# Optimization experiments

Measured on AMD Instinct MI355X. Metric: run time of the kernel, lower is better.

## Reference

```python
import jax, jax.numpy as jnp
import numpy as np

N = 100000
E = 1600000
F_IN, H = 64, 128


def setup_inputs() -> dict:
    key = jax.random.key(0)
    ks = jax.random.split(key, 8)
    inp = {
        "x": jax.random.normal(ks[0], (N, F_IN), dtype=jnp.float32),
        "edge_index": jax.random.randint(ks[1], (2, E), 0, N, dtype=jnp.int64),
        "W1": jax.random.normal(ks[2], (F_IN, H), dtype=jnp.float32) / np.sqrt(F_IN),
        "b1": jnp.zeros((H,), jnp.float32),
        "W2": jax.random.normal(ks[3], (H, H), dtype=jnp.float32) / np.sqrt(H),
        "b2": jnp.zeros((H,), jnp.float32),
        "W3": jax.random.normal(ks[4], (H, H // 2), dtype=jnp.float32) / np.sqrt(H),
        "b3": jnp.zeros((H // 2,), jnp.float32),
        "Wc1": jax.random.normal(ks[5], (H // 2, H // 4), dtype=jnp.float32) / np.sqrt(H // 2),
        "bc1": jnp.zeros((H // 4,), jnp.float32),
        "Wc2": jax.random.normal(ks[6], (H // 4, 2), dtype=jnp.float32) / np.sqrt(H // 4),
        "bc2": jnp.zeros((2,), jnp.float32),
    }
    return inp


def _gcn_norm(edge_index, n):
    # PyG GCNConv default: add self-loops, symmetric D^-1/2 A_hat D^-1/2 norm
    loop = jnp.arange(n, dtype=edge_index.dtype)
    src = jnp.concatenate([edge_index[0], loop])
    dst = jnp.concatenate([edge_index[1], loop])
    deg = jax.ops.segment_sum(jnp.ones_like(dst, dtype=jnp.float32), dst, num_segments=n)
    dis = jax.lax.rsqrt(jnp.maximum(deg, 1.0))
    norm = dis[src] * dis[dst]  # [E+N]
    return src, dst, norm


def _gcn_conv(x, W, b, src, dst, norm, n):
    h = x @ W                      # [N, H_out]
    msg = h[src] * norm[:, None]   # gather + scale, [E+N, H_out]
    out = jax.ops.segment_sum(msg, dst, num_segments=n)  # scatter-add
    return out + b


def reference(x, edge_index, W1, b1, W2, b2, W3, b3, Wc1, bc1, Wc2, bc2):
    n = x.shape[0]
    src, dst, norm = _gcn_norm(edge_index, n)
    h1 = jax.nn.relu(_gcn_conv(x, W1, b1, src, dst, norm, n))
    h2 = jax.nn.relu(_gcn_conv(h1, W2, b2, src, dst, norm, n))
    h3 = jax.nn.relu(_gcn_conv(h2, W3, b3, src, dst, norm, n))
    pooled = jnp.mean(h3, axis=0, keepdims=True)  # [1, H//2]
    z = jax.nn.relu(pooled @ Wc1 + bc1)
    logits = z @ Wc2 + bc2
    return jax.nn.softmax(logits, axis=1)
```

## Files before the change

### kernel.cpp

```cpp
#include <hip/hip_runtime.h>

#define NN 100000
#define NE 1600000
#define NBUCKET 391
#define CHUNK 4096

typedef __attribute__((ext_vector_type(2))) float v2f;
typedef __attribute__((ext_vector_type(8))) short bf16x8;
typedef __attribute__((ext_vector_type(4))) float f32x4;


__device__ __forceinline__ unsigned int pk4fp8(float a, float b, float c, float d) {
    int t = __builtin_amdgcn_cvt_pk_fp8_f32(a, b, 0, false);
    t = __builtin_amdgcn_cvt_pk_fp8_f32(c, d, t, true);
    return (unsigned int)t;
}
__device__ __forceinline__ void acc4(unsigned int u, float* a) {
    v2f p0 = __builtin_amdgcn_cvt_pk_f32_fp8((int)u, false);
    v2f p1 = __builtin_amdgcn_cvt_pk_f32_fp8((int)u, true);
    a[0] += p0.x; a[1] += p0.y; a[2] += p1.x; a[3] += p1.y;
}
__device__ __forceinline__ void acc16(uint4 u, float* a) {
    acc4(u.x, a); acc4(u.y, a + 4); acc4(u.z, a + 8); acc4(u.w, a + 12);
}


__device__ __forceinline__ unsigned short f2b(float f) {
    unsigned int u; __builtin_memcpy(&u, &f, 4);
    unsigned int r = (u + 0x7fffu + ((u >> 16) & 1u)) >> 16;
    return (unsigned short)r;
}
__device__ __forceinline__ unsigned int pk2b(float a, float b) {
    return (unsigned int)f2b(a) | ((unsigned int)f2b(b) << 16);
}

__global__ __launch_bounds__(256) void k_init(
    const float* __restrict__ W1, const float* __restrict__ W2,
    const float* __restrict__ W3, uint4* __restrict__ Wp,
    int* __restrict__ bcnt, int* __restrict__ done_cnt) {
    int t = blockIdx.x * 256 + threadIdx.x;
    if (t < 4096) {
        const float* W; int Dout, e, base;
        if (t < 1024)       { W = W1; Dout = 128; e = t;        base = 0; }
        else if (t < 3072)  { W = W2; Dout = 128; e = t - 1024; base = 1024; }
        else                { W = W3; Dout = 64;  e = t - 3072; base = 3072; }
        int k4q = e / Dout, ch = e % Dout;
        int k0 = (k4q >> 2) * 32 + (k4q & 3) * 8;
        float v[8];
        #pragma unroll
        for (int j = 0; j < 8; j++) v[j] = W[(k0 + j) * Dout + ch];
        uint4 u;
        u.x = pk2b(v[0], v[1]); u.y = pk2b(v[2], v[3]);
        u.z = pk2b(v[4], v[5]); u.w = pk2b(v[6], v[7]);
        Wp[base + e] = u;
    } else {
        int i = t - 4096;
        if (i < NBUCKET) bcnt[i] = 0;
        if (i == NBUCKET) { done_cnt[0] = 0; done_cnt[1] = 0; }
    }
}

__global__ __launch_bounds__(512) void k_p12(const int* __restrict__ dst,
                                             int* __restrict__ bcnt,
                                             int* __restrict__ bbase,
                                             int* __restrict__ bfill,
                                             int* __restrict__ done_cnt, int E) {
    __shared__ int h[NBUCKET];
    __shared__ int s[512];
    __shared__ int isLast;
    int t = threadIdx.x;
    for (int i = t; i < NBUCKET; i += 512) h[i] = 0;
    __syncthreads();
    int stride = gridDim.x * 512;
    for (int i = blockIdx.x * 512 + t; i < E; i += stride)
        atomicAdd(&h[dst[i] >> 8], 1);
    __syncthreads();
    for (int i = t; i < NBUCKET; i += 512)
        if (h[i]) atomicAdd(&bcnt[i], h[i]);
    __threadfence();
    if (t == 0) isLast = (atomicAdd(&done_cnt[0], 1) == (int)gridDim.x - 1);
    __syncthreads();
    if (!isLast) return;
    __threadfence();
    int v = (t < NBUCKET) ? bcnt[t] : 0;
    s[t] = v; __syncthreads();
    for (int off = 1; off < 512; off <<= 1) {
        int x = (t >= off) ? s[t - off] : 0;
        __syncthreads();
        s[t] += x;
        __syncthreads();
    }
    if (t < NBUCKET) { int ex = s[t] - v; bbase[t] = ex; bfill[t] = ex; }
    if (t == NBUCKET) bbase[t] = s[511];
}

__global__ __launch_bounds__(256) void k_p2(const int* __restrict__ src,
                                            const int* __restrict__ dst,
                                            int* __restrict__ bfill,
                                            unsigned int* __restrict__ entries, int E) {
    __shared__ int h[NBUCKET];
    __shared__ int cur[NBUCKET];
    int c0 = blockIdx.x * CHUNK;
    int c1 = min(E, c0 + CHUNK);
    for (int i = threadIdx.x; i < NBUCKET; i += 256) h[i] = 0;
    __syncthreads();
    for (int i = c0 + threadIdx.x; i < c1; i += 256) atomicAdd(&h[dst[i] >> 8], 1);
    __syncthreads();
    for (int i = threadIdx.x; i < NBUCKET; i += 256)
        cur[i] = h[i] ? atomicAdd(&bfill[i], h[i]) : 0;
    __syncthreads();
    for (int i = c0 + threadIdx.x; i < c1; i += 256) {
        int d = dst[i];
        int bkt = d >> 8;
        int pos = atomicAdd(&cur[bkt], 1);
        entries[pos] = (unsigned int)src[i] | ((unsigned int)(d & 255) << 17);
    }
}

__global__ __launch_bounds__(256) void k_p4x(const unsigned int* __restrict__ entries,
                                             const int* __restrict__ bbase,
                                             int* __restrict__ row_ptr,
                                             float* __restrict__ dis,
                                             int* __restrict__ col,
                                             const float4* __restrict__ x4,
                                             uint2* __restrict__ xb2, int N) {
    __shared__ int cnt[256];
    __shared__ int cur[256];
    __shared__ int sc[256];
    __shared__ float sdis[256];
    int b = blockIdx.x;
    int e0 = bbase[b], e1 = bbase[b + 1];
    int t = threadIdx.x;
    cnt[t] = 0; __syncthreads();
    for (int i = e0 + t; i < e1; i += 256)
        atomicAdd(&cnt[(entries[i] >> 17) & 255], 1);
    __syncthreads();
    int v = cnt[t];
    sc[t] = v; __syncthreads();
    for (int off = 1; off < 256; off <<= 1) {
        int x = (t >= off) ? sc[t - off] : 0;
        __syncthreads();
        sc[t] += x;
        __syncthreads();
    }
    int ex = sc[t] - v;
    int n = (b << 8) + t;
    float dv = rsqrtf((float)(v + 1));
    if (n <= N) row_ptr[n] = e0 + ex;
    if (n < N) dis[n] = dv;
    sdis[t] = dv;
    cur[t] = e0 + ex;
    __syncthreads();
    for (int i = e0 + t; i < e1; i += 256) {
        unsigned int en = entries[i];
        int pos = atomicAdd(&cur[(en >> 17) & 255], 1);
        col[pos] = (int)(en & 0x1FFFF);
    }
    for (int idx = t; idx < 256 * 8; idx += 256) {
        int node = idx >> 3, k = idx & 7;
        int gn = (b << 8) + node;
        if (gn < N) {
            float s = sdis[node];
            float4 A = x4[gn * 16 + 2 * k];
            float4 B = x4[gn * 16 + 2 * k + 1];
            uint2 u;
            u.x = pk4fp8(A.x * s, A.y * s, A.z * s, A.w * s);
            u.y = pk4fp8(B.x * s, B.y * s, B.z * s, B.w * s);
            xb2[gn * 8 + k] = u;
        }
    }
}

__global__ __launch_bounds__(256) void k_l1f(
    const uint4* __restrict__ xb4, const int* __restrict__ row_ptr,
    const int* __restrict__ col, const float* __restrict__ dis,
    const uint4* __restrict__ Wp, const float* __restrict__ b1,
    unsigned int* __restrict__ h1u, int N) {
    __shared__ unsigned short lds[4][16][72];
    const int tid = threadIdx.x, lane = tid & 63, wave = tid >> 6;
    const int slot = lane >> 2, seg = lane & 3;
    const int n = blockIdx.x * 64 + wave * 16 + slot;
    float a[16];
    #pragma unroll
    for (int q = 0; q < 16; q++) a[q] = 0.f;
    if (n < N) {
        int b = row_ptr[n], e = row_ptr[n + 1];
        acc16(xb4[n * 4 + seg], a);
        int i = b;
        for (; i + 4 <= e; i += 4) {
            int c0 = col[i], c1 = col[i + 1], c2 = col[i + 2], c3 = col[i + 3];
            uint4 u0 = xb4[c0 * 4 + seg], u1 = xb4[c1 * 4 + seg];
            uint4 u2 = xb4[c2 * 4 + seg], u3 = xb4[c3 * 4 + seg];
            acc16(u0, a); acc16(u1, a); acc16(u2, a); acc16(u3, a);
        }
        for (; i < e; i++) acc16(xb4[col[i] * 4 + seg], a);
        float s = dis[n];
        #pragma unroll
        for (int q = 0; q < 16; q++) a[q] *= s;
    }
    uint4 u0, u1;
    u0.x = pk2b(a[0],  a[1]);  u0.y = pk2b(a[2],  a[3]);
    u0.z = pk2b(a[4],  a[5]);  u0.w = pk2b(a[6],  a[7]);
    u1.x = pk2b(a[8],  a[9]);  u1.y = pk2b(a[10], a[11]);
    u1.z = pk2b(a[12], a[13]); u1.w = pk2b(a[14], a[15]);
    *(uint4*)&lds[wave][slot][seg * 16]     = u0;
    *(uint4*)&lds[wave][slot][seg * 16 + 8] = u1;
    __syncthreads();
    const int quad = lane >> 4, l16 = lane & 15;
    const int node = blockIdx.x * 64 + wave * 16 + l16;
    const bool valid = node < N;
    bf16x8 bfrag[2];
    #pragma unroll
    for (int kt = 0; kt < 2; kt++)
        bfrag[kt] = *(bf16x8*)&lds[wave][l16][kt * 32 + quad * 8];
    const float s2 = valid ? dis[node] : 0.f;
    #pragma unroll
    for (int ct = 0; ct < 8; ct++) {
        f32x4 c = {0.f, 0.f, 0.f, 0.f};
        #pragma unroll
        for (int kt = 0; kt < 2; kt++) {
            uint4 wu = Wp[(kt * 4 + quad) * 128 + ct * 16 + l16];
            c = __builtin_amdgcn_mfma_f32_16x16x32_bf16(*(bf16x8*)&wu, bfrag[kt], c, 0, 0, 0);
        }
        if (valid) {
            const int chb = ct * 16 + quad * 4;
            float r0 = fmaxf(c[0] + b1[chb + 0], 0.f) * s2;
            float r1 = fmaxf(c[1] + b1[chb + 1], 0.f) * s2;
            float r2 = fmaxf(c[2] + b1[chb + 2], 0.f) * s2;
            float r3 = fmaxf(c[3] + b1[chb + 3], 0.f) * s2;
            h1u[(size_t)node * 32 + ct * 4 + quad] = pk4fp8(r0, r1, r2, r3);
        }
    }
}

__global__ __launch_bounds__(256) void k_agg128s(
    const uint4* __restrict__ g4, const int* __restrict__ row_ptr,
    const int* __restrict__ col, const float* __restrict__ dis,
    uint4* __restrict__ outb, int N) {
    int tid = threadIdx.x;
    int lane = tid & 63, wave = tid >> 6;
    int slot = lane >> 3, seg = lane & 7;
    int n = blockIdx.x * 32 + wave * 8 + slot;
    if (n >= N) return;
    int b = row_ptr[n], e = row_ptr[n + 1];
    float a[16];
    #pragma unroll
    for (int q = 0; q < 16; q++) a[q] = 0.f;
    acc16(g4[n * 8 + seg], a);
    int i = b;
    for (; i + 4 <= e; i += 4) {
        int c0 = col[i], c1 = col[i + 1], c2 = col[i + 2], c3 = col[i + 3];
        uint4 u0 = g4[c0 * 8 + seg], u1 = g4[c1 * 8 + seg];
        uint4 u2 = g4[c2 * 8 + seg], u3 = g4[c3 * 8 + seg];
        acc16(u0, a); acc16(u1, a); acc16(u2, a); acc16(u3, a);
    }
    for (; i < e; i++) acc16(g4[col[i] * 8 + seg], a);
    float s = dis[n];
    uint4 u0, u1;
    u0.x = pk2b(s*a[0],  s*a[1]);  u0.y = pk2b(s*a[2],  s*a[3]);
    u0.z = pk2b(s*a[4],  s*a[5]);  u0.w = pk2b(s*a[6],  s*a[7]);
    u1.x = pk2b(s*a[8],  s*a[9]);  u1.y = pk2b(s*a[10], s*a[11]);
    u1.z = pk2b(s*a[12], s*a[13]); u1.w = pk2b(s*a[14], s*a[15]);
    outb[n * 16 + seg * 2]     = u0;
    outb[n * 16 + seg * 2 + 1] = u1;
}

__global__ __launch_bounds__(256) void k_mm23(
    const uint4* __restrict__ Xb,
    const uint4* __restrict__ Wp2, const uint4* __restrict__ Wp3,
    const float* __restrict__ b2, const float* __restrict__ dis,
    unsigned int* __restrict__ g3u, int N) {
    __shared__ unsigned short lds[4][16][136];
    const int tid = threadIdx.x, lane = tid & 63, wave = tid >> 6;
    const int quad = lane >> 4, l16 = lane & 15;
    const int node = blockIdx.x * 64 + wave * 16 + l16;
    const bool valid = node < N;
    const int nc = valid ? node : (N - 1);
    bf16x8 bfrag[4];
    const uint4* xrow = Xb + (size_t)nc * 16;
    #pragma unroll
    for (int kt = 0; kt < 4; kt++) {
        uint4 u = xrow[kt * 4 + quad];
        bfrag[kt] = *(bf16x8*)&u;
    }
    const float s = valid ? dis[node] : 0.f;
    #pragma unroll
    for (int ct = 0; ct < 8; ct++) {
        f32x4 c = {0.f, 0.f, 0.f, 0.f};
        #pragma unroll
        for (int kt = 0; kt < 4; kt++) {
            uint4 wu = Wp2[(kt * 4 + quad) * 128 + ct * 16 + l16];
            c = __builtin_amdgcn_mfma_f32_16x16x32_bf16(*(bf16x8*)&wu, bfrag[kt], c, 0, 0, 0);
        }
        const int chb = ct * 16 + quad * 4;
        float r0 = fmaxf(c[0] + b2[chb + 0], 0.f) * s;
        float r1 = fmaxf(c[1] + b2[chb + 1], 0.f) * s;
        float r2 = fmaxf(c[2] + b2[chb + 2], 0.f) * s;
        float r3 = fmaxf(c[3] + b2[chb + 3], 0.f) * s;
        uint2 u; u.x = pk2b(r0, r1); u.y = pk2b(r2, r3);
        *(uint2*)&lds[wave][l16][chb] = u;
    }
    __syncthreads();
    bf16x8 b2frag[4];
    #pragma unroll
    for (int kt = 0; kt < 4; kt++)
        b2frag[kt] = *(bf16x8*)&lds[wave][l16][kt * 32 + quad * 8];
    #pragma unroll
    for (int ct = 0; ct < 4; ct++) {
        f32x4 c = {0.f, 0.f, 0.f, 0.f};
        #pragma unroll
        for (int kt = 0; kt < 4; kt++) {
            uint4 wu = Wp3[(kt * 4 + quad) * 64 + ct * 16 + l16];
            c = __builtin_amdgcn_mfma_f32_16x16x32_bf16(*(bf16x8*)&wu, b2frag[kt], c, 0, 0, 0);
        }
        if (valid)
            g3u[(size_t)node * 16 + ct * 4 + quad] = pk4fp8(c[0], c[1], c[2], c[3]);
    }
}

__global__ __launch_bounds__(256) void k_aggpools(
    const uint4* __restrict__ g4, const int* __restrict__ row_ptr,
    const int* __restrict__ col, const float* __restrict__ dis,
    const float* __restrict__ b3, float* __restrict__ partial, int N) {
    int tid = threadIdx.x;
    int lane = tid & 63, wave = tid >> 6;
    int slot = lane >> 2, seg = lane & 3;
    int n = blockIdx.x * 64 + wave * 16 + slot;
    float ap[16];
    #pragma unroll
    for (int j = 0; j < 16; j++) ap[j] = 0.f;
    if (n < N) {
        int b = row_ptr[n], e = row_ptr[n + 1];
        float a[16];
        #pragma unroll
        for (int q = 0; q < 16; q++) a[q] = 0.f;
        acc16(g4[n * 4 + seg], a);
        int i = b;
        for (; i + 4 <= e; i += 4) {
            int c0 = col[i], c1 = col[i + 1], c2 = col[i + 2], c3 = col[i + 3];
            uint4 u0 = g4[c0 * 4 + seg], u1 = g4[c1 * 4 + seg];
            uint4 u2 = g4[c2 * 4 + seg], u3 = g4[c3 * 4 + seg];
            acc16(u0, a); acc16(u1, a); acc16(u2, a); acc16(u3, a);
        }
        for (; i < e; i++) acc16(g4[col[i] * 4 + seg], a);
        float s = dis[n];
        #pragma unroll
        for (int j = 0; j < 16; j++)
            ap[j] = fmaxf(s * a[j] + b3[seg * 16 + j], 0.f);
    }
    #pragma unroll
    for (int j = 0; j < 16; j++) {
        ap[j] += __shfl_xor(ap[j], 4);
        ap[j] += __shfl_xor(ap[j], 8);
        ap[j] += __shfl_xor(ap[j], 16);
        ap[j] += __shfl_xor(ap[j], 32);
    }
    __shared__ float red[4][64];
    if (slot == 0) {
        #pragma unroll
        for (int j = 0; j < 16; j++) red[wave][seg * 16 + j] = ap[j];
    }
    __syncthreads();
    if (tid < 64)
        partial[blockIdx.x * 64 + tid] =
            red[0][tid] + red[1][tid] + red[2][tid] + red[3][tid];
}

__global__ __launch_bounds__(256) void k_redhead(
    const float* __restrict__ partial, float* __restrict__ partial2,
    const float* __restrict__ Wc1, const float* __restrict__ bc1,
    const float* __restrict__ Wc2, const float* __restrict__ bc2,
    float* __restrict__ out, int* __restrict__ done_cnt,
    int NB, int NRED, float invN) {
    __shared__ float red[256];
    __shared__ float pooled[64];
    __shared__ float z[32];
    __shared__ float lg[2];
    __shared__ int isLast;
    int blk = blockIdx.x, t = threadIdx.x;
    int lane = t & 63, grp = t >> 6;
    int start = blk * 16, end = min(NB, start + 16);
    float s = 0.f;
    for (int b = start + grp; b < end; b += 4) s += partial[b * 64 + lane];
    red[t] = s; __syncthreads();
    if (t < 64)
        partial2[blk * 64 + t] = red[t] + red[t + 64] + red[t + 128] + red[t + 192];
    __threadfence();
    if (t == 0) isLast = (atomicAdd(done_cnt, 1) == NRED - 1);
    __syncthreads();
    if (!isLast) return;
    __threadfence();
    float s2 = 0.f;
    for (int b = grp; b < NRED; b += 4) s2 += partial2[b * 64 + lane];
    red[t] = s2; __syncthreads();
    if (t < 64) pooled[t] = (red[t] + red[t + 64] + red[t + 128] + red[t + 192]) * invN;
    __syncthreads();
    if (t < 32) {
        float a = bc1[t];
        for (int l = 0; l < 64; l++) a += pooled[l] * Wc1[l * 32 + t];
        z[t] = fmaxf(a, 0.f);
    }
    __syncthreads();
    if (t < 2) {
        float a = bc2[t];
        for (int j = 0; j < 32; j++) a += z[j] * Wc2[j * 2 + t];
        lg[t] = a;
    }
    __syncthreads();
    if (t == 0) {
        float m = fmaxf(lg[0], lg[1]);
        float e0 = __expf(lg[0] - m), e1 = __expf(lg[1] - m);
        float inv = 1.f / (e0 + e1);
        out[0] = e0 * inv;
        out[1] = e1 * inv;
    }
}


extern "C" void kernel_launch(void* const* d_in, const int* in_sizes, int n_in,
                              void* d_out, int out_size, void* d_ws, size_t ws_size,
                              hipStream_t stream) {
    (void)in_sizes; (void)n_in; (void)out_size; (void)ws_size;
    const int N = NN, E = NE;

    const float* x   = (const float*)d_in[0];
    const int*   ei  = (const int*)d_in[1];
    const int*   srcp = ei;
    const int*   dstp = ei + E;
    const float* W1 = (const float*)d_in[2];
    const float* b1 = (const float*)d_in[3];
    const float* W2 = (const float*)d_in[4];
    const float* b2 = (const float*)d_in[5];
    const float* W3 = (const float*)d_in[6];
    const float* b3 = (const float*)d_in[7];
    const float* Wc1 = (const float*)d_in[8];
    const float* bc1 = (const float*)d_in[9];
    const float* Wc2 = (const float*)d_in[10];
    const float* bc2 = (const float*)d_in[11];
    float* out = (float*)d_out;

    char* base = (char*)d_ws;
    size_t off = 0;
    auto carve = [&](size_t bytes) -> char* {
        char* p = base + off;
        off = (off + bytes + 255) & ~(size_t)255;
        return p;
    };
    int*   bcnt    = (int*)carve((size_t)NBUCKET * 4);
    int*   bbase   = (int*)carve((size_t)(NBUCKET + 1) * 4);
    int*   bfill   = (int*)carve((size_t)NBUCKET * 4);
    int*   done_cnt= (int*)carve(256);
    int*   row_ptr = (int*)carve((size_t)(N + 1) * 4);
    int*   col     = (int*)carve((size_t)E * 4);
    float* dis     = (float*)carve((size_t)N * 4);
    float* partial = (float*)carve((size_t)1600 * 64 * 4);
    float* partial2= (float*)carve((size_t)128 * 64 * 4);
    uint4* Wp      = (uint4*)carve((size_t)4096 * 16);
    unsigned int* entries = (unsigned int*)carve((size_t)E * 4);
    unsigned int* xb      = (unsigned int*)carve((size_t)N * 64);
    unsigned int* h1u     = (unsigned int*)carve((size_t)N * 128);
    unsigned int* g3u     = (unsigned int*)carve((size_t)N * 64);
    uint4*        bufB    = (uint4*)carve((size_t)N * 128 * 2);

    k_init<<<18, 256, 0, stream>>>(W1, W2, W3, Wp, bcnt, done_cnt);
    k_p12<<<256, 512, 0, stream>>>(dstp, bcnt, bbase, bfill, &done_cnt[0], E);
    k_p2<<<(E + CHUNK - 1) / CHUNK, 256, 0, stream>>>(srcp, dstp, bfill, entries, E);
    k_p4x<<<NBUCKET, 256, 0, stream>>>(entries, bbase, row_ptr, dis, col,
                                       (const float4*)x, (uint2*)xb, N);

    const int NB64 = (N + 63) / 64;
    const int NB32 = (N + 31) / 32;

    k_l1f<<<NB64, 256, 0, stream>>>((const uint4*)xb, row_ptr, col, dis, Wp, b1, h1u, N);

    k_agg128s<<<NB32, 256, 0, stream>>>((const uint4*)h1u, row_ptr, col, dis, bufB, N);
    k_mm23<<<NB64, 256, 0, stream>>>(bufB, Wp + 1024, Wp + 3072, b2, dis, g3u, N);

    k_aggpools<<<NB64, 256, 0, stream>>>((const uint4*)g3u, row_ptr, col, dis, b3, partial, N);

    const int NRED = (NB64 + 15) / 16;
    k_redhead<<<NRED, 256, 0, stream>>>(partial, partial2, Wc1, bc1, Wc2, bc2,
                                        out, &done_cnt[1], NB64, NRED, 1.0f / (float)N);
}
```

Baseline: 311.8 us.

## Fuse layer-2 aggregation into matmul kernel via LDS, split histogram/scan kernels

```diff
diff --git a/kernel.cpp b/kernel.cpp
--- a/kernel.cpp
+++ b/kernel.cpp
@@ -60,28 +60,24 @@
     }
 }
 
-__global__ __launch_bounds__(512) void k_p12(const int* __restrict__ dst,
-                                             int* __restrict__ bcnt,
-                                             int* __restrict__ bbase,
-                                             int* __restrict__ bfill,
-                                             int* __restrict__ done_cnt, int E) {
+
+__global__ __launch_bounds__(256) void k_p1(const int* __restrict__ dst,
+                                            int* __restrict__ bcnt, int E) {
     __shared__ int h[NBUCKET];
+    for (int i = threadIdx.x; i < NBUCKET; i += 256) h[i] = 0;
+    __syncthreads();
+    int stride = gridDim.x * 256;
+    for (int i = blockIdx.x * 256 + threadIdx.x; i < E; i += stride)
+        atomicAdd(&h[dst[i] >> 8], 1);
+    __syncthreads();
+    for (int i = threadIdx.x; i < NBUCKET; i += 256)
+        if (h[i]) atomicAdd(&bcnt[i], h[i]);
+}
+
+__global__ void k_scanb(const int* __restrict__ bcnt, int* __restrict__ bbase,
+                        int* __restrict__ bfill) {
     __shared__ int s[512];
-    __shared__ int isLast;
     int t = threadIdx.x;
-    for (int i = t; i < NBUCKET; i += 512) h[i] = 0;
-    __syncthreads();
-    int stride = gridDim.x * 512;
-    for (int i = blockIdx.x * 512 + t; i < E; i += stride)
-        atomicAdd(&h[dst[i] >> 8], 1);
-    __syncthreads();
-    for (int i = t; i < NBUCKET; i += 512)
-        if (h[i]) atomicAdd(&bcnt[i], h[i]);
-    __threadfence();
-    if (t == 0) isLast = (atomicAdd(&done_cnt[0], 1) == (int)gridDim.x - 1);
-    __syncthreads();
-    if (!isLast) return;
-    __threadfence();
     int v = (t < NBUCKET) ? bcnt[t] : 0;
     s[t] = v; __syncthreads();
     for (int off = 1; off < 512; off <<= 1) {
@@ -233,56 +229,54 @@
     }
 }
 
-__global__ __launch_bounds__(256) void k_agg128s(
-    const uint4* __restrict__ g4, const int* __restrict__ row_ptr,
+__global__ __launch_bounds__(256) void k_l2f(
+    const uint4* __restrict__ h1b4, const int* __restrict__ row_ptr,
     const int* __restrict__ col, const float* __restrict__ dis,
-    uint4* __restrict__ outb, int N) {
-    int tid = threadIdx.x;
-    int lane = tid & 63, wave = tid >> 6;
-    int slot = lane >> 3, seg = lane & 7;
-    int n = blockIdx.x * 32 + wave * 8 + slot;
-    if (n >= N) return;
-    int b = row_ptr[n], e = row_ptr[n + 1];
-    float a[16];
-    #pragma unroll
-    for (int q = 0; q < 16; q++) a[q] = 0.f;
-    acc16(g4[n * 8 + seg], a);
-    int i = b;
-    for (; i + 4 <= e; i += 4) {
-        int c0 = col[i], c1 = col[i + 1], c2 = col[i + 2], c3 = col[i + 3];
-        uint4 u0 = g4[c0 * 8 + seg], u1 = g4[c1 * 8 + seg];
-        uint4 u2 = g4[c2 * 8 + seg], u3 = g4[c3 * 8 + seg];
-        acc16(u0, a); acc16(u1, a); acc16(u2, a); acc16(u3, a);
-    }
-    for (; i < e; i++) acc16(g4[col[i] * 8 + seg], a);
-    float s = dis[n];
-    uint4 u0, u1;
-    u0.x = pk2b(s*a[0],  s*a[1]);  u0.y = pk2b(s*a[2],  s*a[3]);
-    u0.z = pk2b(s*a[4],  s*a[5]);  u0.w = pk2b(s*a[6],  s*a[7]);
-    u1.x = pk2b(s*a[8],  s*a[9]);  u1.y = pk2b(s*a[10], s*a[11]);
-    u1.z = pk2b(s*a[12], s*a[13]); u1.w = pk2b(s*a[14], s*a[15]);
-    outb[n * 16 + seg * 2]     = u0;
-    outb[n * 16 + seg * 2 + 1] = u1;
-}
-
-__global__ __launch_bounds__(256) void k_mm23(
-    const uint4* __restrict__ Xb,
     const uint4* __restrict__ Wp2, const uint4* __restrict__ Wp3,
-    const float* __restrict__ b2, const float* __restrict__ dis,
+    const float* __restrict__ b2,
     unsigned int* __restrict__ g3u, int N) {
     __shared__ unsigned short lds[4][16][136];
     const int tid = threadIdx.x, lane = tid & 63, wave = tid >> 6;
+    const int slot = lane >> 3, seg = lane & 7;
+    #pragma unroll
+    for (int j = 0; j < 2; j++) {
+        const int nl = wave * 16 + j * 8 + slot;
+        const int n = blockIdx.x * 64 + nl;
+        float a[16];
+        #pragma unroll
+        for (int q = 0; q < 16; q++) a[q] = 0.f;
+        if (n < N) {
+            int b = row_ptr[n], e = row_ptr[n + 1];
+            acc16(h1b4[(size_t)n * 8 + seg], a);
+            int i = b;
+            for (; i + 4 <= e; i += 4) {
+                int c0 = col[i], c1 = col[i + 1], c2 = col[i + 2], c3 = col[i + 3];
+                uint4 u0 = h1b4[(size_t)c0 * 8 + seg], u1 = h1b4[(size_t)c1 * 8 + seg];
+                uint4 u2 = h1b4[(size_t)c2 * 8 + seg], u3 = h1b4[(size_t)c3 * 8 + seg];
+                acc16(u0, a); acc16(u1, a); acc16(u2, a); acc16(u3, a);
+            }
+            for (; i < e; i++) acc16(h1b4[(size_t)col[i] * 8 + seg], a);
+            float s = dis[n];
+            #pragma unroll
+            for (int q = 0; q < 16; q++) a[q] *= s;
+        }
+        uint4 u0, u1;
+        u0.x = pk2b(a[0],  a[1]);  u0.y = pk2b(a[2],  a[3]);
+        u0.z = pk2b(a[4],  a[5]);  u0.w = pk2b(a[6],  a[7]);
+        u1.x = pk2b(a[8],  a[9]);  u1.y = pk2b(a[10], a[11]);
+        u1.z = pk2b(a[12], a[13]); u1.w = pk2b(a[14], a[15]);
+        const int lnl = j * 8 + slot;
+        *(uint4*)&lds[wave][lnl][seg * 16]     = u0;
+        *(uint4*)&lds[wave][lnl][seg * 16 + 8] = u1;
+    }
+    __syncthreads();
     const int quad = lane >> 4, l16 = lane & 15;
     const int node = blockIdx.x * 64 + wave * 16 + l16;
     const bool valid = node < N;
-    const int nc = valid ? node : (N - 1);
     bf16x8 bfrag[4];
-    const uint4* xrow = Xb + (size_t)nc * 16;
-    #pragma unroll
-    for (int kt = 0; kt < 4; kt++) {
-        uint4 u = xrow[kt * 4 + quad];
-        bfrag[kt] = *(bf16x8*)&u;
-    }
+    #pragma unroll
+    for (int kt = 0; kt < 4; kt++)
+        bfrag[kt] = *(bf16x8*)&lds[wave][l16][kt * 32 + quad * 8];
     const float s = valid ? dis[node] : 0.f;
     #pragma unroll
     for (int ct = 0; ct < 8; ct++) {
@@ -460,21 +454,20 @@
     unsigned int* xb      = (unsigned int*)carve((size_t)N * 64);
     unsigned int* h1u     = (unsigned int*)carve((size_t)N * 128);
     unsigned int* g3u     = (unsigned int*)carve((size_t)N * 64);
-    uint4*        bufB    = (uint4*)carve((size_t)N * 128 * 2);
 
     k_init<<<18, 256, 0, stream>>>(W1, W2, W3, Wp, bcnt, done_cnt);
-    k_p12<<<256, 512, 0, stream>>>(dstp, bcnt, bbase, bfill, &done_cnt[0], E);
+    k_p1<<<512, 256, 0, stream>>>(dstp, bcnt, E);
+    k_scanb<<<1, 512, 0, stream>>>(bcnt, bbase, bfill);
     k_p2<<<(E + CHUNK - 1) / CHUNK, 256, 0, stream>>>(srcp, dstp, bfill, entries, E);
     k_p4x<<<NBUCKET, 256, 0, stream>>>(entries, bbase, row_ptr, dis, col,
                                        (const float4*)x, (uint2*)xb, N);
 
     const int NB64 = (N + 63) / 64;
-    const int NB32 = (N + 31) / 32;
 
     k_l1f<<<NB64, 256, 0, stream>>>((const uint4*)xb, row_ptr, col, dis, Wp, b1, h1u, N);
 
-    k_agg128s<<<NB32, 256, 0, stream>>>((const uint4*)h1u, row_ptr, col, dis, bufB, N);
-    k_mm23<<<NB64, 256, 0, stream>>>(bufB, Wp + 1024, Wp + 3072, b2, dis, g3u, N);
+    k_l2f<<<NB64, 256, 0, stream>>>((const uint4*)h1u, row_ptr, col, dis,
+                                    Wp + 1024, Wp + 3072, b2, g3u, N);
 
     k_aggpools<<<NB64, 256, 0, stream>>>((const uint4*)g3u, row_ptr, col, dis, b3, partial, N);
 
```

Result: faster. 283.5 us (-9.1%).
